# Optimization experiments

Hardware: AMD Instinct MI355X
Metric: run time of the kernel (lower is better)

Reference implementation:

```python
import jax, jax.numpy as jnp
import numpy as np
from jax import lax

N_CLASSES = 10
N_EXPERTS = 45  # 10 choose 2
EPS = 1e-5

# lookup table: (i1, i2) with i1 < i2 -> flat expert id (matches nested loop order)
_tbl = np.zeros((N_CLASSES, N_CLASSES), dtype=np.int32)
_k = 0
for _i1 in range(N_CLASSES):
    for _i2 in range(_i1 + 1, N_CLASSES):
        _tbl[_i1, _i2] = _k
        _k += 1
PAIR_TABLE = jnp.asarray(_tbl)


def _downscale(x):
    # AvgPool2d(3, stride=3) on 28x28 -> 9x9 (floor: uses top-left 27x27)
    B = x.shape[0]
    return x[:, :, :27, :27].reshape(B, 1, 9, 3, 9, 3).mean(axis=(3, 5))


def _bn_eval(h, gamma, beta, mean, var):
    scale = gamma * lax.rsqrt(var + EPS)
    return h * scale[None, :, None, None] + (beta - mean * scale)[None, :, None, None]


def _stage1(x, w1, b1, g1, be1, m1, v1, fcw1, fcb1):
    xd = _downscale(x)                                         # [B,1,9,9]
    h = lax.conv_general_dilated(xd, w1, (1, 1), 'VALID',
                                 dimension_numbers=('NCHW', 'OIHW', 'NCHW'))
    h = h + b1[None, :, None, None]                            # [B,20,7,7]
    h = _bn_eval(h, g1, be1, m1, v1)
    h = jax.nn.relu(h)
    B = h.shape[0]
    h = h[:, :, :6, :6].reshape(B, 20, 3, 2, 3, 2).max(axis=(3, 5))  # maxpool2 -> [B,20,3,3]
    h = h.reshape(B, 180)
    return h @ fcw1.T + fcb1                                   # [B,10] raw logits


def reference(x, w1, b1, g1, be1, m1, v1, fcw1, fcb1,
              w2, b2, g2, be2, m2, v2, fcw2, fcb2):
    B = x.shape[0]
    logits1 = _stage1(x, w1, b1, g1, be1, m1, v1, fcw1, fcb1)  # [B,10]
    ls1 = jax.nn.log_softmax(logits1, axis=1)

    # routing: top-2 class indices, sorted ascending, -> pairwise expert id
    top2 = jnp.sort(jnp.argsort(ls1, axis=1)[:, -2:], axis=1)  # [B,2]
    idx0, idx1 = top2[:, 0], top2[:, 1]
    eid = PAIR_TABLE[idx0, idx1]                               # [B]

    # stage 2 (TinyNet2) with per-example gathered expert params
    xd = _downscale(x)                                         # [B,1,9,9]
    # extract 5x5 conv patches (valid, stride 1): output spatial 5x5
    patches = jnp.stack([xd[:, 0, i:i + 5, j:j + 5]
                         for i in range(5) for j in range(5)], axis=1)  # [B,25,5,5]
    Wsel = w2.reshape(N_EXPERTS, 15, 25)[eid]                  # [B,15,25]
    h = jnp.einsum('bkhw,bok->bohw', patches, Wsel) + b2[eid][:, :, None, None]  # [B,15,5,5]
    scale = (g2 * lax.rsqrt(v2 + EPS))[eid]                    # [B,15]
    shift = (be2 - m2 * g2 * lax.rsqrt(v2 + EPS))[eid]
    h = h * scale[:, :, None, None] + shift[:, :, None, None]
    h = jax.nn.relu(h)
    h = h[:, :, :4, :4].reshape(B, 15, 2, 2, 2, 2).max(axis=(3, 5))  # [B,15,2,2]
    feat = h.reshape(B, 60)
    s2 = jnp.einsum('bf,bof->bo', feat, fcw2[eid]) + fcb2[eid]  # [B,2]

    # combine: scatter the two expert logits into the routed columns
    rows = jnp.arange(B)
    out = jnp.full((B, N_CLASSES), -100.0, dtype=logits1.dtype)
    out = out.at[rows, idx0].set(s2[:, 0]).at[rows, idx1].set(s2[:, 1])
    # eval-mode bypass: use stage1 raw logits if max log-prob > 0.3
    use1 = jnp.max(ls1, axis=1) > 0.3
    out = jnp.where(use1[:, None], logits1, out)
    out = jax.nn.log_softmax(out, axis=1)
    return (logits1, out)


def setup_inputs() -> dict:
    key = jax.random.key(0)
    ks = jax.random.split(key, 18)
    B = 65536
    s = 0.1
    return {
        'x': jax.random.normal(ks[0], (B, 1, 28, 28), dtype=jnp.float32),
        # stage1 (TinyNet, 20 kernels, k=3)
        'w1': jax.random.normal(ks[1], (20, 1, 3, 3), dtype=jnp.float32) * s,
        'b1': jax.random.normal(ks[2], (20,), dtype=jnp.float32) * s,
        'g1': jax.random.normal(ks[3], (20,), dtype=jnp.float32) * s + 1.0,
        'be1': jax.random.normal(ks[4], (20,), dtype=jnp.float32) * s,
        'm1': jax.random.normal(ks[5], (20,), dtype=jnp.float32) * s,
        'v1': jax.random.uniform(ks[6], (20,), dtype=jnp.float32) + 0.5,
        'fcw1': jax.random.normal(ks[7], (10, 180), dtype=jnp.float32) * s,
        'fcb1': jax.random.normal(ks[8], (10,), dtype=jnp.float32) * s,
        # 45 stacked stage2 experts (TinyNet2, 15 kernels, k=5)
        'w2': jax.random.normal(ks[9], (45, 15, 1, 5, 5), dtype=jnp.float32) * s,
        'b2': jax.random.normal(ks[10], (45, 15), dtype=jnp.float32) * s,
        'g2': jax.random.normal(ks[11], (45, 15), dtype=jnp.float32) * s + 1.0,
        'be2': jax.random.normal(ks[12], (45, 15), dtype=jnp.float32) * s,
        'm2': jax.random.normal(ks[13], (45, 15), dtype=jnp.float32) * s,
        'v2': jax.random.uniform(ks[14], (45, 15), dtype=jnp.float32) + 0.5,
        'fcw2': jax.random.normal(ks[15], (45, 2, 60), dtype=jnp.float32) * s,
        'fcb2': jax.random.normal(ks[16], (45, 2), dtype=jnp.float32) * s,
    }
```

## Files before the change

### kernel.cpp

```cpp
#include <hip/hip_runtime.h>
#include <cmath>

#define EPSF 1e-5f


__global__ __launch_bounds__(256) void setup_tables(
    const float* __restrict__ w1, const float* __restrict__ b1,
    const float* __restrict__ g1, const float* __restrict__ be1,
    const float* __restrict__ m1, const float* __restrict__ v1,
    const float* __restrict__ w2, const float* __restrict__ b2,
    const float* __restrict__ g2, const float* __restrict__ be2,
    const float* __restrict__ m2, const float* __restrict__ v2,
    const float* __restrict__ fcw2, const float* __restrict__ fcb2,
    float* __restrict__ ws, int B)
{
  const int t  = blockIdx.x * blockDim.x + threadIdx.x;
  const int nt = gridDim.x * blockDim.x;
  float* W2F  = ws + (size_t)B * 84;
  float* B2F  = W2F + 18900;
  float* FC2  = W2F + 19576;
  float* FCB2 = FC2 + 5400;
  float* W1F  = FCB2 + 90;
  float* B1F  = W1F + 180;

  for (int idx = t; idx < 18900; idx += nt) {
    int kk = idx & 3, rest = idx >> 2;
    int e = rest % 45, ok4 = rest / 45;
    int k4 = ok4 % 7, o = ok4 / 7;
    int k = k4 * 4 + kk;
    float s = g2[e*15+o] / sqrtf(v2[e*15+o] + EPSF);
    W2F[idx] = (k < 25) ? w2[(e*15+o)*25 + k] * s : 0.0f;
  }
  for (int idx = t; idx < 675; idx += nt) {
    int e = idx % 45, o = idx / 45;
    float s = g2[e*15+o] / sqrtf(v2[e*15+o] + EPSF);
    B2F[idx] = b2[e*15+o]*s + be2[e*15+o] - m2[e*15+o]*s;
  }
  for (int idx = t; idx < 5400; idx += nt) {
    int kk = idx & 3, rest = idx >> 2;
    int e = rest % 45, t2 = rest / 45;
    int f4 = t2 % 15, oo = t2 / 15;
    FC2[idx] = fcw2[(e*2+oo)*60 + f4*4 + kk];
  }
  for (int idx = t; idx < 90; idx += nt) {
    int e = idx % 45, oo = idx / 45;
    FCB2[idx] = fcb2[e*2+oo];
  }
  for (int idx = t; idx < 180; idx += nt) {
    int ch = idx / 9;
    float s = g1[ch] / sqrtf(v1[ch] + EPSF);
    W1F[idx] = w1[idx] * s;
  }
  for (int idx = t; idx < 20; idx += nt) {
    float s = g1[idx] / sqrtf(v1[idx] + EPSF);
    B1F[idx] = b1[idx]*s + be1[idx] - m1[idx]*s;
  }
}

__global__ __launch_bounds__(256) void downscale_k(
    const float* __restrict__ x, float* __restrict__ ws, int B)
{
  int t = blockIdx.x * blockDim.x + threadIdx.x;
  if (t >= B * 27) return;
  int trip = t % 3;
  int br   = t / 3;
  int r = br % 9;
  int b = br / 9;
  const float* xb = x + (size_t)b * 784;
  float s0 = 0.f, s1 = 0.f, s2 = 0.f;
  #pragma unroll
  for (int dr = 0; dr < 3; dr++) {
    const float* row = xb + (3*r + dr) * 28;
    const float4* rv = reinterpret_cast<const float4*>(row) + 2*trip;
    float4 A = rv[0], Bv = rv[1], Cv = rv[2];
    if (trip == 0)      { s0 += A.x+A.y+A.z;  s1 += A.w+Bv.x+Bv.y;  s2 += Bv.z+Bv.w+Cv.x; }
    else if (trip == 1) { s0 += A.y+A.z+A.w;  s1 += Bv.x+Bv.y+Bv.z; s2 += Bv.w+Cv.x+Cv.y; }
    else                { s0 += A.z+A.w+Bv.x; s1 += Bv.y+Bv.z+Bv.w; s2 += Cv.x+Cv.y+Cv.z; }
  }
  float* xdp = ws + (size_t)b * 84 + r * 9 + 3 * trip;
  xdp[0] = s0 / 9.0f; xdp[1] = s1 / 9.0f; xdp[2] = s2 / 9.0f;
}

__global__ __launch_bounds__(256) void main_k(
    const float* __restrict__ ws,
    const float* __restrict__ fcw1, const float* __restrict__ fcb1,
    float* __restrict__ out, int B)
{
  int b = blockIdx.x * blockDim.x + threadIdx.x;
  if (b >= B) return;

  const float* W2F  = ws + (size_t)B * 84;
  const float* B2F  = W2F + 18900;
  const float* FC2  = W2F + 19576;
  const float* FCB2 = FC2 + 5400;
  const float* W1F  = FCB2 + 90;
  const float* B1F  = W1F + 180;

  float xd[81];
  {
    const float* xdp = ws + (size_t)b * 84;
    const float4* xv = reinterpret_cast<const float4*>(xdp);
    #pragma unroll
    for (int i = 0; i < 20; i++) {
      float4 v = xv[i];
      xd[4*i+0] = v.x; xd[4*i+1] = v.y; xd[4*i+2] = v.z; xd[4*i+3] = v.w;
    }
    xd[80] = xdp[80];
  }

  float logits[10];
  #pragma unroll
  for (int c = 0; c < 10; c++) logits[c] = fcb1[c];

  #pragma unroll 1
  for (int ch = 0; ch < 20; ch++) {
    float w[9];
    #pragma unroll
    for (int k = 0; k < 9; k++) w[k] = W1F[ch*9 + k];
    float bb = B1F[ch];
    float feat[9];
    #pragma unroll
    for (int pr = 0; pr < 3; pr++) {
      #pragma unroll
      for (int pc = 0; pc < 3; pc++) {
        float c00 = bb, c01 = bb, c10 = bb, c11 = bb;
        #pragma unroll
        for (int dr = 0; dr < 3; dr++) {
          #pragma unroll
          for (int dc = 0; dc < 3; dc++) {
            float wk = w[dr*3 + dc];
            c00 = fmaf(xd[(2*pr+0+dr)*9 + 2*pc+0+dc], wk, c00);
            c01 = fmaf(xd[(2*pr+0+dr)*9 + 2*pc+1+dc], wk, c01);
            c10 = fmaf(xd[(2*pr+1+dr)*9 + 2*pc+0+dc], wk, c10);
            c11 = fmaf(xd[(2*pr+1+dr)*9 + 2*pc+1+dc], wk, c11);
          }
        }
        feat[pr*3+pc] = fmaxf(fmaxf(fmaxf(c00, c01), fmaxf(c10, c11)), 0.0f);
      }
    }
    #pragma unroll
    for (int c = 0; c < 10; c++) {
      float acc = logits[c];
      #pragma unroll
      for (int p = 0; p < 9; p++)
        acc = fmaf(feat[p], fcw1[c*180 + ch*9 + p], acc);
      logits[c] = acc;
    }
  }

  int i1 = 0; float v1m = logits[0];
  #pragma unroll
  for (int c = 1; c < 10; c++) { if (logits[c] >= v1m) { v1m = logits[c]; i1 = c; } }
  int i2 = 0; float v2m = -3.0e38f;
  #pragma unroll
  for (int c = 0; c < 10; c++) { if (c != i1 && logits[c] >= v2m) { v2m = logits[c]; i2 = c; } }
  int idx0 = i1 < i2 ? i1 : i2;
  int idx1 = i1 < i2 ? i2 : i1;
  int eid  = 8*idx0 - (idx0*(idx0-1))/2 + idx1 - 1;

  float mx = v1m;
  float sume = 0.0f;
  #pragma unroll
  for (int c = 0; c < 10; c++) sume += expf(logits[c] - mx);
  bool use1 = (-logf(sume)) > 0.3f;

  const float4* W2F4 = reinterpret_cast<const float4*>(W2F);
  const float4* FC24 = reinterpret_cast<const float4*>(FC2);

  float s2a = FCB2[eid], s2b = FCB2[45 + eid];

  float4 wv[7], fa, fb; float bias;
  #pragma unroll
  for (int k4 = 0; k4 < 7; k4++) wv[k4] = W2F4[k4*45 + eid];
  bias = B2F[eid];
  fa = FC24[eid];
  fb = FC24[15*45 + eid];

  #pragma unroll 1
  for (int o = 0; o < 15; o++) {
    float4 nwv[7], nfa, nfb; float nbias;
    if (o < 14) {
      #pragma unroll
      for (int k4 = 0; k4 < 7; k4++) nwv[k4] = W2F4[((o+1)*7 + k4)*45 + eid];
      nbias = B2F[(o+1)*45 + eid];
      nfa = FC24[(o+1)*45 + eid];
      nfb = FC24[(15 + o+1)*45 + eid];
    }
    float wr[28];
    #pragma unroll
    for (int k4 = 0; k4 < 7; k4++) {
      wr[4*k4+0] = wv[k4].x; wr[4*k4+1] = wv[k4].y;
      wr[4*k4+2] = wv[k4].z; wr[4*k4+3] = wv[k4].w;
    }
    float feat0 = 0.f, feat1 = 0.f, feat2 = 0.f, feat3 = 0.f;
    #pragma unroll
    for (int ph = 0; ph < 2; ph++) {
      #pragma unroll
      for (int pw = 0; pw < 2; pw++) {
        float c00 = bias, c01 = bias, c10 = bias, c11 = bias;
        #pragma unroll
        for (int i = 0; i < 5; i++) {
          #pragma unroll
          for (int j = 0; j < 5; j++) {
            float wk = wr[i*5 + j];
            c00 = fmaf(xd[(2*ph+0+i)*9 + 2*pw+0+j], wk, c00);
            c01 = fmaf(xd[(2*ph+0+i)*9 + 2*pw+1+j], wk, c01);
            c10 = fmaf(xd[(2*ph+1+i)*9 + 2*pw+0+j], wk, c10);
            c11 = fmaf(xd[(2*ph+1+i)*9 + 2*pw+1+j], wk, c11);
          }
        }
        float f = fmaxf(fmaxf(fmaxf(c00, c01), fmaxf(c10, c11)), 0.0f);
        if (ph == 0 && pw == 0) feat0 = f;
        else if (ph == 0)       feat1 = f;
        else if (pw == 0)       feat2 = f;
        else                    feat3 = f;
      }
    }
    s2a = fmaf(feat0, fa.x, fmaf(feat1, fa.y, fmaf(feat2, fa.z, fmaf(feat3, fa.w, s2a))));
    s2b = fmaf(feat0, fb.x, fmaf(feat1, fb.y, fmaf(feat2, fb.z, fmaf(feat3, fb.w, s2b))));
    if (o < 14) {
      #pragma unroll
      for (int k4 = 0; k4 < 7; k4++) wv[k4] = nwv[k4];
      bias = nbias; fa = nfa; fb = nfb;
    }
  }

  float o10[10];
  #pragma unroll
  for (int c = 0; c < 10; c++) {
    float v = -100.0f;
    v = (c == idx0) ? s2a : v;
    v = (c == idx1) ? s2b : v;
    o10[c] = use1 ? logits[c] : v;
  }
  float m2x = o10[0];
  #pragma unroll
  for (int c = 1; c < 10; c++) m2x = fmaxf(m2x, o10[c]);
  float se2 = 0.0f;
  #pragma unroll
  for (int c = 0; c < 10; c++) se2 += expf(o10[c] - m2x);
  float lse2 = m2x + logf(se2);

  size_t base = (size_t)b * 10;
  #pragma unroll
  for (int c = 0; c < 10; c++) out[base + c] = logits[c];
  #pragma unroll
  for (int c = 0; c < 10; c++) out[(size_t)B*10 + base + c] = o10[c] - lse2;
}

extern "C" void kernel_launch(void* const* d_in, const int* in_sizes, int n_in,
                              void* d_out, int out_size, void* d_ws, size_t ws_size,
                              hipStream_t stream) {
  const float* x    = (const float*)d_in[0];
  const float* w1   = (const float*)d_in[1];
  const float* b1   = (const float*)d_in[2];
  const float* g1   = (const float*)d_in[3];
  const float* be1  = (const float*)d_in[4];
  const float* m1   = (const float*)d_in[5];
  const float* v1   = (const float*)d_in[6];
  const float* fcw1 = (const float*)d_in[7];
  const float* fcb1 = (const float*)d_in[8];
  const float* w2   = (const float*)d_in[9];
  const float* b2   = (const float*)d_in[10];
  const float* g2   = (const float*)d_in[11];
  const float* be2  = (const float*)d_in[12];
  const float* m2   = (const float*)d_in[13];
  const float* v2   = (const float*)d_in[14];
  const float* fcw2 = (const float*)d_in[15];
  const float* fcb2 = (const float*)d_in[16];
  float* out = (float*)d_out;
  float* ws  = (float*)d_ws;
  const int B = in_sizes[0] / 784;

  setup_tables<<<80, 256, 0, stream>>>(w1, b1, g1, be1, m1, v1,
                                       w2, b2, g2, be2, m2, v2, fcw2, fcb2, ws, B);
  const int nds = B * 27;
  downscale_k<<<(nds + 255)/256, 256, 0, stream>>>(x, ws, B);
  main_k<<<(B + 255)/256, 256, 0, stream>>>(ws, fcw1, fcb1, out, B);
}
```

Baseline: 401.4 us.

## Fuse downscale into main kernel via shared memory, shrink blocks to 64

Removes the separate downscale kernel and its global workspace round-trip: each 64-thread block now pools its 64 samples into shared memory (padded stride 85) and then runs the per-sample network from there. Block size drops from 256 to 64 to match the per-block shared staging, and the weight-register copy array is replaced by direct float4 component selection. This saves a kernel launch and global traffic, but the downscale loop's index math assumes B is a multiple of 64 (it reads samples past B in the last block), and shared-memory reads at stride 85 may bank-conflict.

```diff
diff --git a/kernel.cpp b/kernel.cpp
--- a/kernel.cpp
+++ b/kernel.cpp
@@ -12,11 +12,11 @@
     const float* __restrict__ g2, const float* __restrict__ be2,
     const float* __restrict__ m2, const float* __restrict__ v2,
     const float* __restrict__ fcw2, const float* __restrict__ fcb2,
-    float* __restrict__ ws, int B)
+    float* __restrict__ ws)
 {
   const int t  = blockIdx.x * blockDim.x + threadIdx.x;
   const int nt = gridDim.x * blockDim.x;
-  float* W2F  = ws + (size_t)B * 84;
+  float* W2F  = ws;
   float* B2F  = W2F + 18900;
   float* FC2  = W2F + 19576;
   float* FCB2 = FC2 + 5400;
@@ -57,39 +57,45 @@
   }
 }
 
-__global__ __launch_bounds__(256) void downscale_k(
-    const float* __restrict__ x, float* __restrict__ ws, int B)
-{
-  int t = blockIdx.x * blockDim.x + threadIdx.x;
-  if (t >= B * 27) return;
-  int trip = t % 3;
-  int br   = t / 3;
-  int r = br % 9;
-  int b = br / 9;
-  const float* xb = x + (size_t)b * 784;
-  float s0 = 0.f, s1 = 0.f, s2 = 0.f;
-  #pragma unroll
-  for (int dr = 0; dr < 3; dr++) {
-    const float* row = xb + (3*r + dr) * 28;
-    const float4* rv = reinterpret_cast<const float4*>(row) + 2*trip;
-    float4 A = rv[0], Bv = rv[1], Cv = rv[2];
-    if (trip == 0)      { s0 += A.x+A.y+A.z;  s1 += A.w+Bv.x+Bv.y;  s2 += Bv.z+Bv.w+Cv.x; }
-    else if (trip == 1) { s0 += A.y+A.z+A.w;  s1 += Bv.x+Bv.y+Bv.z; s2 += Bv.w+Cv.x+Cv.y; }
-    else                { s0 += A.z+A.w+Bv.x; s1 += Bv.y+Bv.z+Bv.w; s2 += Cv.x+Cv.y+Cv.z; }
-  }
-  float* xdp = ws + (size_t)b * 84 + r * 9 + 3 * trip;
-  xdp[0] = s0 / 9.0f; xdp[1] = s1 / 9.0f; xdp[2] = s2 / 9.0f;
-}
-
-__global__ __launch_bounds__(256) void main_k(
+#define WK4(arr, k) ((k)%4==0 ? arr[(k)/4].x : (k)%4==1 ? arr[(k)/4].y : \
+                     (k)%4==2 ? arr[(k)/4].z : arr[(k)/4].w)
+
+__global__ __launch_bounds__(64) void fused_k(
+    const float* __restrict__ x,
     const float* __restrict__ ws,
     const float* __restrict__ fcw1, const float* __restrict__ fcb1,
     float* __restrict__ out, int B)
 {
-  int b = blockIdx.x * blockDim.x + threadIdx.x;
+  __shared__ float sxd[64 * 85];
+  const int tid = threadIdx.x;
+  const int b0  = blockIdx.x * 64;
+
+  #pragma unroll 1
+  for (int it = 0; it < 27; it++) {
+    int idx  = it * 64 + tid;
+    int trip = idx % 3;
+    int r    = (idx / 3) % 9;
+    int s    = idx / 27;
+    const float* xb = x + (size_t)(b0 + s) * 784;
+    float s0 = 0.f, s1 = 0.f, s2 = 0.f;
+    #pragma unroll
+    for (int dr = 0; dr < 3; dr++) {
+      const float* row = xb + (3*r + dr) * 28;
+      const float4* rv = reinterpret_cast<const float4*>(row) + 2*trip;
+      float4 A = rv[0], Bv = rv[1], Cv = rv[2];
+      if (trip == 0)      { s0 += A.x+A.y+A.z;  s1 += A.w+Bv.x+Bv.y;  s2 += Bv.z+Bv.w+Cv.x; }
+      else if (trip == 1) { s0 += A.y+A.z+A.w;  s1 += Bv.x+Bv.y+Bv.z; s2 += Bv.w+Cv.x+Cv.y; }
+      else                { s0 += A.z+A.w+Bv.x; s1 += Bv.y+Bv.z+Bv.w; s2 += Cv.x+Cv.y+Cv.z; }
+    }
+    float* xdp = &sxd[s*85 + r*9 + 3*trip];
+    xdp[0] = s0 / 9.0f; xdp[1] = s1 / 9.0f; xdp[2] = s2 / 9.0f;
+  }
+  __syncthreads();
+
+  const int b = b0 + tid;
   if (b >= B) return;
 
-  const float* W2F  = ws + (size_t)B * 84;
+  const float* W2F  = ws;
   const float* B2F  = W2F + 18900;
   const float* FC2  = W2F + 19576;
   const float* FCB2 = FC2 + 5400;
@@ -98,14 +104,9 @@
 
   float xd[81];
   {
-    const float* xdp = ws + (size_t)b * 84;
-    const float4* xv = reinterpret_cast<const float4*>(xdp);
-    #pragma unroll
-    for (int i = 0; i < 20; i++) {
-      float4 v = xv[i];
-      xd[4*i+0] = v.x; xd[4*i+1] = v.y; xd[4*i+2] = v.z; xd[4*i+3] = v.w;
-    }
-    xd[80] = xdp[80];
+    const float* p = &sxd[tid * 85];
+    #pragma unroll
+    for (int k = 0; k < 81; k++) xd[k] = p[k];
   }
 
   float logits[10];
@@ -186,12 +187,6 @@
       nfa = FC24[(o+1)*45 + eid];
       nfb = FC24[(15 + o+1)*45 + eid];
     }
-    float wr[28];
-    #pragma unroll
-    for (int k4 = 0; k4 < 7; k4++) {
-      wr[4*k4+0] = wv[k4].x; wr[4*k4+1] = wv[k4].y;
-      wr[4*k4+2] = wv[k4].z; wr[4*k4+3] = wv[k4].w;
-    }
     float feat0 = 0.f, feat1 = 0.f, feat2 = 0.f, feat3 = 0.f;
     #pragma unroll
     for (int ph = 0; ph < 2; ph++) {
@@ -202,7 +197,7 @@
         for (int i = 0; i < 5; i++) {
           #pragma unroll
           for (int j = 0; j < 5; j++) {
-            float wk = wr[i*5 + j];
+            float wk = WK4(wv, i*5 + j);
             c00 = fmaf(xd[(2*ph+0+i)*9 + 2*pw+0+j], wk, c00);
             c01 = fmaf(xd[(2*ph+0+i)*9 + 2*pw+1+j], wk, c01);
             c10 = fmaf(xd[(2*ph+1+i)*9 + 2*pw+0+j], wk, c10);
@@ -273,8 +268,6 @@
   const int B = in_sizes[0] / 784;
 
   setup_tables<<<80, 256, 0, stream>>>(w1, b1, g1, be1, m1, v1,
-                                       w2, b2, g2, be2, m2, v2, fcw2, fcb2, ws, B);
-  const int nds = B * 27;
-  downscale_k<<<(nds + 255)/256, 256, 0, stream>>>(x, ws, B);
-  main_k<<<(B + 255)/256, 256, 0, stream>>>(ws, fcw1, fcb1, out, B);
+                                       w2, b2, g2, be2, m2, v2, fcw2, fcb2, ws);
+  fused_k<<<(B + 63)/64, 64, 0, stream>>>(x, ws, fcw1, fcb1, out, B);
 }
```

Result: slower. 415.3 us (+3.5%).

## Transpose downscaled images to feature-major layout and shrink main kernel blocks

Applied to the files above, without the earlier changes.

The downscaled 9x9 images are now stored feature-major (k*B + b) instead of per-example rows of 84 floats, so loads in the main kernel are coalesced across threads. The main kernel drops to 64-thread blocks with launch_bounds(64,1), giving more blocks and a larger register budget per thread. The weight register array copy is replaced by direct float4 component access. Risks are more strided stores in the downscale kernel and lower occupancy per CU.

```diff
diff --git a/kernel.cpp b/kernel.cpp
--- a/kernel.cpp
+++ b/kernel.cpp
@@ -16,7 +16,7 @@
 {
   const int t  = blockIdx.x * blockDim.x + threadIdx.x;
   const int nt = gridDim.x * blockDim.x;
-  float* W2F  = ws + (size_t)B * 84;
+  float* W2F  = ws + (size_t)81 * B;
   float* B2F  = W2F + 18900;
   float* FC2  = W2F + 19576;
   float* FCB2 = FC2 + 5400;
@@ -62,10 +62,10 @@
 {
   int t = blockIdx.x * blockDim.x + threadIdx.x;
   if (t >= B * 27) return;
-  int trip = t % 3;
-  int br   = t / 3;
-  int r = br % 9;
-  int b = br / 9;
+  int j = t % 27;
+  int b = t / 27;
+  int trip = j % 3;
+  int r    = j / 3;
   const float* xb = x + (size_t)b * 784;
   float s0 = 0.f, s1 = 0.f, s2 = 0.f;
   #pragma unroll
@@ -77,19 +77,24 @@
     else if (trip == 1) { s0 += A.y+A.z+A.w;  s1 += Bv.x+Bv.y+Bv.z; s2 += Bv.w+Cv.x+Cv.y; }
     else                { s0 += A.z+A.w+Bv.x; s1 += Bv.y+Bv.z+Bv.w; s2 += Cv.x+Cv.y+Cv.z; }
   }
-  float* xdp = ws + (size_t)b * 84 + r * 9 + 3 * trip;
-  xdp[0] = s0 / 9.0f; xdp[1] = s1 / 9.0f; xdp[2] = s2 / 9.0f;
-}
-
-__global__ __launch_bounds__(256) void main_k(
+  const int k0 = r * 9 + 3 * trip;
+  ws[(size_t)(k0+0) * B + b] = s0 * (1.0f/9.0f);
+  ws[(size_t)(k0+1) * B + b] = s1 * (1.0f/9.0f);
+  ws[(size_t)(k0+2) * B + b] = s2 * (1.0f/9.0f);
+}
+
+#define GETC(arr, k) ((k)%4==0 ? arr[(k)/4].x : (k)%4==1 ? arr[(k)/4].y : \
+                      (k)%4==2 ? arr[(k)/4].z : arr[(k)/4].w)
+
+__global__ __launch_bounds__(64, 1) void main_k(
     const float* __restrict__ ws,
     const float* __restrict__ fcw1, const float* __restrict__ fcb1,
     float* __restrict__ out, int B)
 {
-  int b = blockIdx.x * blockDim.x + threadIdx.x;
+  const int b = blockIdx.x * 64 + threadIdx.x;
   if (b >= B) return;
 
-  const float* W2F  = ws + (size_t)B * 84;
+  const float* W2F  = ws + (size_t)81 * B;
   const float* B2F  = W2F + 18900;
   const float* FC2  = W2F + 19576;
   const float* FCB2 = FC2 + 5400;
@@ -98,14 +103,9 @@
 
   float xd[81];
   {
-    const float* xdp = ws + (size_t)b * 84;
-    const float4* xv = reinterpret_cast<const float4*>(xdp);
-    #pragma unroll
-    for (int i = 0; i < 20; i++) {
-      float4 v = xv[i];
-      xd[4*i+0] = v.x; xd[4*i+1] = v.y; xd[4*i+2] = v.z; xd[4*i+3] = v.w;
-    }
-    xd[80] = xdp[80];
+    const float* p = ws + b;
+    #pragma unroll
+    for (int k = 0; k < 81; k++) xd[k] = p[(size_t)k * B];
   }
 
   float logits[10];
@@ -186,12 +186,6 @@
       nfa = FC24[(o+1)*45 + eid];
       nfb = FC24[(15 + o+1)*45 + eid];
     }
-    float wr[28];
-    #pragma unroll
-    for (int k4 = 0; k4 < 7; k4++) {
-      wr[4*k4+0] = wv[k4].x; wr[4*k4+1] = wv[k4].y;
-      wr[4*k4+2] = wv[k4].z; wr[4*k4+3] = wv[k4].w;
-    }
     float feat0 = 0.f, feat1 = 0.f, feat2 = 0.f, feat3 = 0.f;
     #pragma unroll
     for (int ph = 0; ph < 2; ph++) {
@@ -202,7 +196,7 @@
         for (int i = 0; i < 5; i++) {
           #pragma unroll
           for (int j = 0; j < 5; j++) {
-            float wk = wr[i*5 + j];
+            float wk = GETC(wv, i*5 + j);
             c00 = fmaf(xd[(2*ph+0+i)*9 + 2*pw+0+j], wk, c00);
             c01 = fmaf(xd[(2*ph+0+i)*9 + 2*pw+1+j], wk, c01);
             c10 = fmaf(xd[(2*ph+1+i)*9 + 2*pw+0+j], wk, c10);
@@ -276,5 +270,5 @@
                                        w2, b2, g2, be2, m2, v2, fcw2, fcb2, ws, B);
   const int nds = B * 27;
   downscale_k<<<(nds + 255)/256, 256, 0, stream>>>(x, ws, B);
-  main_k<<<(B + 255)/256, 256, 0, stream>>>(ws, fcw1, fcb1, out, B);
-}
+  main_k<<<(B + 63)/64, 64, 0, stream>>>(ws, fcw1, fcb1, out, B);
+}
```

Result: slower. 422.6 us (+5.3%).
